# Kernel tuning notes

Measured on AMD Instinct MI355X. Metric: run time of the kernel, lower is better.

## Reference

```python
import jax, jax.numpy as jnp
import numpy as np

KH, KW = 3, 3
STRIDE, PAD, DIL = 1, 1, 1


def setup_inputs() -> dict:
    key = jax.random.key(0)
    k1, k2, k3, k4 = jax.random.split(key, 4)
    B, C, H, W = 4, 256, 64, 64
    O = 256
    x = jax.random.normal(k1, (B, C, H, W), dtype=jnp.float32)
    offset = jax.random.normal(k2, (B, 2 * KH * KW, H, W), dtype=jnp.float32)
    mask = jax.random.uniform(k3, (B, KH * KW, H, W), dtype=jnp.float32)
    weight = jax.random.normal(k4, (O, C, KH, KW), dtype=jnp.float32) * 0.02
    bias = jnp.zeros((O,), dtype=jnp.float32)
    return {"x": x, "offset": offset, "mask": mask, "weight": weight, "bias": bias}


def _bilinear_sample(x, py, px):
    # x: [B,C,H,W]; py,px: [B,K,Ho,Wo] fractional sample coords (zero outside)
    B, C, H, W = x.shape
    y0 = jnp.floor(py)
    x0 = jnp.floor(px)
    ly, lx = py - y0, px - x0
    hy, hx = 1.0 - ly, 1.0 - lx
    y0i = y0.astype(jnp.int32)
    x0i = x0.astype(jnp.int32)
    xf = x.reshape(B, C, H * W)

    def gather(yi, xi):
        valid = (yi >= 0) & (yi < H) & (xi >= 0) & (xi < W)
        yc = jnp.clip(yi, 0, H - 1)
        xc = jnp.clip(xi, 0, W - 1)
        idx = yc * W + xc  # [B,K,Ho,Wo]
        g = jax.vmap(lambda xb, ib: xb[:, ib.reshape(-1)])(xf, idx)  # [B,C,K*Ho*Wo]
        g = g.reshape(B, C, *yi.shape[1:])
        return g * valid[:, None].astype(x.dtype)

    return (gather(y0i, x0i) * (hy * hx)[:, None]
            + gather(y0i, x0i + 1) * (hy * lx)[:, None]
            + gather(y0i + 1, x0i) * (ly * hx)[:, None]
            + gather(y0i + 1, x0i + 1) * (ly * lx)[:, None])


def reference(x, offset, mask, weight, bias):
    B, C, H, W = x.shape
    O = weight.shape[0]
    K = KH * KW
    Ho = (H + 2 * PAD - DIL * (KH - 1) - 1) // STRIDE + 1
    Wo = (W + 2 * PAD - DIL * (KW - 1) - 1) // STRIDE + 1
    off = offset.reshape(B, K, 2, Ho, Wo)
    tap_y = (jnp.repeat(jnp.arange(KH), KW) * DIL).astype(x.dtype)  # [K]
    tap_x = (jnp.tile(jnp.arange(KW), KH) * DIL).astype(x.dtype)
    base_y = (jnp.arange(Ho) * STRIDE - PAD).astype(x.dtype)  # [Ho]
    base_x = (jnp.arange(Wo) * STRIDE - PAD).astype(x.dtype)
    py = off[:, :, 0] + base_y[None, None, :, None] + tap_y[None, :, None, None]
    px = off[:, :, 1] + base_x[None, None, None, :] + tap_x[None, :, None, None]
    # sampled columns: [B,C,K,Ho,Wo], modulated by mask
    val = _bilinear_sample(x, py, px) * mask[:, None]
    out = jnp.einsum('bckhw,ock->bohw', val, weight.reshape(O, C, K))
    return out + bias[None, :, None, None]
```

## Files before the change

### kernel.cpp

```cpp
#include <hip/hip_runtime.h>

typedef _Float16 f16x8 __attribute__((ext_vector_type(8)));
typedef float f32x4 __attribute__((ext_vector_type(4)));

__device__ __forceinline__ unsigned short f2h(float f) {
  union { _Float16 h; unsigned short u; } v;
  v.h = (_Float16)f;
  return v.u;
}
__device__ __forceinline__ f16x8 splat8(float w) {
  _Float16 h = (_Float16)w;
  f16x8 v = {h, h, h, h, h, h, h, h};
  return v;
}

__global__ __launch_bounds__(256) void prep_wx(
    const float* __restrict__ x, const float* __restrict__ w,
    unsigned short* __restrict__ xt, uint4* __restrict__ wfrag) {
  const int bid = blockIdx.x;
  const int t = threadIdx.x;
  if (bid >= 1024) {
    const int idx = (bid - 1024) * 256 + t;
    const int l = idx & 63;
    const int kt = (idx >> 6) % 72;
    const int g = idx / (72 * 64);
    const int o = g * 16 + (l & 15);
    const int kbase = kt * 32 + ((l >> 4) * 8);
    unsigned short h[8];
#pragma unroll
    for (int e = 0; e < 8; ++e) {
      const int klin = kbase + e;
      const int kk = klin >> 8;
      const int c = klin & 255;
      h[e] = f2h(w[((size_t)o * 256 + c) * 9 + kk]);
    }
    uint4 p;
    p.x = (unsigned)h[0] | ((unsigned)h[1] << 16);
    p.y = (unsigned)h[2] | ((unsigned)h[3] << 16);
    p.z = (unsigned)h[4] | ((unsigned)h[5] << 16);
    p.w = (unsigned)h[6] | ((unsigned)h[7] << 16);
    wfrag[idx] = p;
    return;
  }
  const int b = bid >> 8;
  const int h = (bid >> 2) & 63;
  const int cq = bid & 3;
  const int wave = t >> 6, lane = t & 63;
  __shared__ float lds[64][65];
  const int wpos = t >> 2, sub = t & 3;
  const int cl0 = wave * 4 + (lane >> 4);
  const int w0 = (lane & 15) * 4;
#pragma unroll
  for (int iter = 0; iter < 4; ++iter) {
    const int cl = iter * 16 + cl0;
    const int c = cq * 64 + cl;
    float4 v = *(const float4*)(x + (((size_t)b * 256 + c) * 64 + h) * 64 + w0);
    lds[cl][w0] = v.x; lds[cl][w0 + 1] = v.y;
    lds[cl][w0 + 2] = v.z; lds[cl][w0 + 3] = v.w;
  }
  __syncthreads();
  unsigned short hb[16];
#pragma unroll
  for (int j = 0; j < 16; ++j) hb[j] = f2h(lds[sub * 16 + j][wpos]);
  uint4 p0, p1;
  p0.x = (unsigned)hb[0] | ((unsigned)hb[1] << 16);
  p0.y = (unsigned)hb[2] | ((unsigned)hb[3] << 16);
  p0.z = (unsigned)hb[4] | ((unsigned)hb[5] << 16);
  p0.w = (unsigned)hb[6] | ((unsigned)hb[7] << 16);
  p1.x = (unsigned)hb[8] | ((unsigned)hb[9] << 16);
  p1.y = (unsigned)hb[10] | ((unsigned)hb[11] << 16);
  p1.z = (unsigned)hb[12] | ((unsigned)hb[13] << 16);
  p1.w = (unsigned)hb[14] | ((unsigned)hb[15] << 16);
  unsigned short* dst = xt + (((size_t)b * 64 + h) * 64 + wpos) * 256 + cq * 64 + sub * 16;
  *(uint4*)dst = p0;
  *(uint4*)(dst + 8) = p1;
}

__device__ __forceinline__ void combine8(uint4 q0, uint4 q1, uint4 q2, uint4 q3,
                                         float4 wt, _Float16* dst) {
  f16x8 t0, t1, t2, t3;
  __builtin_memcpy(&t0, &q0, 16);
  __builtin_memcpy(&t1, &q1, 16);
  __builtin_memcpy(&t2, &q2, 16);
  __builtin_memcpy(&t3, &q3, 16);
  f16x8 r = t0 * splat8(wt.x);
  r += t1 * splat8(wt.y);
  r += t2 * splat8(wt.z);
  r += t3 * splat8(wt.w);
  __builtin_memcpy(dst, &r, 16);
}

__global__ __launch_bounds__(512, 2) void dcn_fused(
    const unsigned short* __restrict__ xt, const float* __restrict__ off,
    const float* __restrict__ mask, const uint4* __restrict__ wfrag,
    const float* __restrict__ bias, float* __restrict__ out) {
  __shared__ __align__(16) _Float16 Bs[2][4096];
  __shared__ __align__(16) float swt[9 * 64 * 4];
  __shared__ __align__(16) int sidx[9 * 64 * 4];

  const int bid = blockIdx.x;
  const int id = ((bid & 7) << 5) | (bid >> 3);
  const int b = id >> 6;
  const int nt = id & 63;

  const int tid = threadIdx.x;
  const int lane = tid & 63;
  const int wv = tid >> 6;
  const int lh = lane & 15, lg = lane >> 4;

  for (int pair = tid; pair < 576; pair += 512) {
    const int k = pair >> 6;
    const int pl = pair & 63;
    float oy = off[(((size_t)b * 18 + 2 * k) * 64 + nt) * 64 + pl];
    float ox = off[(((size_t)b * 18 + 2 * k + 1) * 64 + nt) * 64 + pl];
    float m = mask[(((size_t)b * 9 + k) * 64 + nt) * 64 + pl];
    float py = oy + (float)(nt - 1 + k / 3);
    float px = ox + (float)(pl - 1 + k % 3);
    float y0f = floorf(py), x0f = floorf(px);
    float ly = py - y0f, lx = px - x0f;
    float hy = 1.f - ly, hx = 1.f - lx;
    int y0 = (int)y0f, x0 = (int)x0f;
    int y1 = y0 + 1, x1 = x0 + 1;
    bool vy0 = (y0 >= 0) && (y0 < 64);
    bool vy1 = (y1 >= 0) && (y1 < 64);
    bool vx0 = (x0 >= 0) && (x0 < 64);
    bool vx1 = (x1 >= 0) && (x1 < 64);
    int yc0 = min(max(y0, 0), 63), yc1 = min(max(y1, 0), 63);
    int xc0 = min(max(x0, 0), 63), xc1 = min(max(x1, 0), 63);
    int* sp = sidx + (k * 64 + pl) * 4;
    float* wp = swt + (k * 64 + pl) * 4;
    sp[0] = (yc0 * 64 + xc0) * 256;
    sp[1] = (yc0 * 64 + xc1) * 256;
    sp[2] = (yc1 * 64 + xc0) * 256;
    sp[3] = (yc1 * 64 + xc1) * 256;
    wp[0] = (vy0 && vx0) ? hy * hx * m : 0.f;
    wp[1] = (vy0 && vx1) ? hy * lx * m : 0.f;
    wp[2] = (vy1 && vx0) ? ly * hx * m : 0.f;
    wp[3] = (vy1 && vx1) ? ly * lx * m : 0.f;
  }

  const uint4* aBase = wfrag + (size_t)(wv * 2) * 72 * 64 + lane;

  const int pos = tid >> 3, ci = tid & 7;
  const unsigned short* xtb = xt + (size_t)b * 1048576 + ci * 8;
  const int bsw = (ci >> 2) * 2048 + pos * 32 + (((ci & 3) ^ ((pos >> 1) & 3)) * 8);

  const int csw = (lg ^ ((lh >> 1) & 3)) * 8;
  int boff[4];
#pragma unroll
  for (int fn = 0; fn < 4; ++fn) boff[fn] = (fn * 16 + lh) * 32 + csw;

#define LOADA(P, AR)                                                               \
  do {                                                                             \
    _Pragma("unroll") for (int j = 0; j < 4; ++j)                                  \
        AR[j] = aBase[(size_t)((((j & 1) * 72) + 2 * (P) + (j >> 1)) * 64)];       \
  } while (0)

#define LOADTAPS(Q0, Q1, Q2, Q3, IX, CO)                                           \
  do {                                                                             \
    Q0 = *(const uint4*)(xtb + (IX).x + (CO));                                     \
    Q1 = *(const uint4*)(xtb + (IX).y + (CO));                                     \
    Q2 = *(const uint4*)(xtb + (IX).z + (CO));                                     \
    Q3 = *(const uint4*)(xtb + (IX).w + (CO));                                     \
  } while (0)

#define MFMA_PHASE(BUF, AR)                                                        \
  do {                                                                             \
    const _Float16* Bb = &Bs[BUF][0];                                              \
    f16x8 b0[4], b1[4];                                                            \
    _Pragma("unroll") for (int fn = 0; fn < 4; ++fn) {                             \
      b0[fn] = *(const f16x8*)(Bb + boff[fn]);                                     \
      b1[fn] = *(const f16x8*)(Bb + 2048 + boff[fn]);                              \
    }                                                                              \
    __builtin_amdgcn_s_setprio(1);                                                 \
    _Pragma("unroll") for (int fm = 0; fm < 2; ++fm)                               \
        _Pragma("unroll") for (int fn = 0; fn < 4; ++fn) {                         \
      acc[fm][fn] = __builtin_amdgcn_mfma_f32_16x16x32_f16(                        \
          *(const f16x8*)&AR[fm], b0[fn], acc[fm][fn], 0, 0, 0);                   \
      acc[fm][fn] = __builtin_amdgcn_mfma_f32_16x16x32_f16(                        \
          *(const f16x8*)&AR[2 + fm], b1[fn], acc[fm][fn], 0, 0, 0);               \
    }                                                                              \
    __builtin_amdgcn_s_setprio(0);                                                 \
  } while (0)

#define BAR()                                                                      \
  do {                                                                             \
    asm volatile("s_waitcnt lgkmcnt(0)" ::: "memory");                             \
    __builtin_amdgcn_sched_barrier(0);                                             \
    __builtin_amdgcn_s_barrier();                                                  \
    __builtin_amdgcn_sched_barrier(0);                                             \
  } while (0)

#define PHASE(P_, AL, AC, QL0, QL1, QL2, QL3, QC0, QC1, QC2, QC3)                  \
  do {                                                                             \
    LOADA((P_) + 1, AL);                                                           \
    int4 ix = *(const int4*)(sidx + ((((P_) + 2) >> 2) * 64 + pos) * 4);           \
    LOADTAPS(QL0, QL1, QL2, QL3, ix, (((P_) + 2) & 3) * 64);                       \
    MFMA_PHASE((P_) & 1, AC);                                                      \
    float4 wt4 = *(const float4*)(swt + ((((P_) + 1) >> 2) * 64 + pos) * 4);       \
    combine8(QC0, QC1, QC2, QC3, wt4, &Bs[((P_) + 1) & 1][0] + bsw);               \
    BAR();                                                                         \
  } while (0)

  f32x4 acc[2][4] = {};
  uint4 AE[4], AO[4];
  uint4 qA0, qA1, qA2, qA3, qB0, qB1, qB2, qB3;

  __syncthreads();

  {
    float4 wt0 = *(const float4*)(swt + pos * 4);
    int4 ix0 = *(const int4*)(sidx + pos * 4);
    LOADTAPS(qA0, qA1, qA2, qA3, ix0, 0);
    combine8(qA0, qA1, qA2, qA3, wt0, &Bs[0][0] + bsw);
    LOADA(0, AE);
    LOADTAPS(qB0, qB1, qB2, qB3, ix0, 64);
    BAR();
  }

  for (int p = 0; p < 34; p += 2) {
    PHASE(p, AO, AE, qA0, qA1, qA2, qA3, qB0, qB1, qB2, qB3);
    PHASE(p + 1, AE, AO, qB0, qB1, qB2, qB3, qA0, qA1, qA2, qA3);
  }
  {
    LOADA(35, AO);
    float4 wt4 = *(const float4*)(swt + (8 * 64 + pos) * 4);
    MFMA_PHASE(0, AE);
    combine8(qB0, qB1, qB2, qB3, wt4, &Bs[1][0] + bsw);
    BAR();
    MFMA_PHASE(1, AO);
  }

  float* outb = out + (size_t)b * 1048576 + (size_t)nt * 64;
#pragma unroll
  for (int fm = 0; fm < 2; ++fm) {
#pragma unroll
    for (int i = 0; i < 4; ++i) {
      const int o = wv * 32 + fm * 16 + lg * 4 + i;
      const float bs = bias[o];
      float* orow = outb + (size_t)o * 4096 + lh;
#pragma unroll
      for (int fn = 0; fn < 4; ++fn) orow[fn * 16] = acc[fm][fn][i] + bs;
    }
  }
#undef LOADA
#undef LOADTAPS
#undef MFMA_PHASE
#undef BAR
#undef PHASE
}

extern "C" void kernel_launch(void* const* d_in, const int* in_sizes, int n_in,
                              void* d_out, int out_size, void* d_ws, size_t ws_size,
                              hipStream_t stream) {
  const float* x = (const float*)d_in[0];
  const float* off = (const float*)d_in[1];
  const float* mask = (const float*)d_in[2];
  const float* wgt = (const float*)d_in[3];
  const float* bias = (const float*)d_in[4];
  float* out = (float*)d_out;

  uint4* wfrag = (uint4*)d_ws;
  unsigned short* xtp = (unsigned short*)(wfrag + 73728);

  prep_wx<<<1312, 256, 0, stream>>>(x, wgt, xtp, wfrag);
  dcn_fused<<<256, 512, 0, stream>>>(xtp, off, mask, wfrag, bias, out);
}
```

Baseline: 45.98 us.

## Split K across wave halves with 64x64 warp tiles and LDS reduction

Changes the wave-to-tile mapping so that 4 waves each own 64 output channels and two wave groups split each K step. Each wave now loads one B fragment set and 4 A fragments instead of two B halves and 2x2 A fragments, which improves reuse of the B data read from LDS per MFMA. The partial sums are reduced through shared memory (dynamic, 68 KB) before the store. Extra costs are a larger accumulator register footprint, an LDS reduction pass with two barriers, and higher shared memory per block, which may hurt occupancy at 2 blocks per CU.

```diff
diff --git a/kernel.cpp b/kernel.cpp
--- a/kernel.cpp
+++ b/kernel.cpp
@@ -94,9 +94,11 @@
     const unsigned short* __restrict__ xt, const float* __restrict__ off,
     const float* __restrict__ mask, const uint4* __restrict__ wfrag,
     const float* __restrict__ bias, float* __restrict__ out) {
-  __shared__ __align__(16) _Float16 Bs[2][4096];
-  __shared__ __align__(16) float swt[9 * 64 * 4];
-  __shared__ __align__(16) int sidx[9 * 64 * 4];
+  extern __shared__ char smem[];
+  _Float16* Bs = (_Float16*)smem;
+  float* swt = (float*)(smem + 16384);
+  int* sidx = (int*)(smem + 25600);
+  float* red = (float*)smem;
 
   const int bid = blockIdx.x;
   const int id = ((bid & 7) << 5) | (bid >> 3);
@@ -106,6 +108,8 @@
   const int tid = threadIdx.x;
   const int lane = tid & 63;
   const int wv = tid >> 6;
+  const int m = wv & 3;
+  const int ks = wv >> 2;
   const int lh = lane & 15, lg = lane >> 4;
 
   for (int pair = tid; pair < 576; pair += 512) {
@@ -113,7 +117,7 @@
     const int pl = pair & 63;
     float oy = off[(((size_t)b * 18 + 2 * k) * 64 + nt) * 64 + pl];
     float ox = off[(((size_t)b * 18 + 2 * k + 1) * 64 + nt) * 64 + pl];
-    float m = mask[(((size_t)b * 9 + k) * 64 + nt) * 64 + pl];
+    float mk = mask[(((size_t)b * 9 + k) * 64 + nt) * 64 + pl];
     float py = oy + (float)(nt - 1 + k / 3);
     float px = ox + (float)(pl - 1 + k % 3);
     float y0f = floorf(py), x0f = floorf(px);
@@ -133,13 +137,13 @@
     sp[1] = (yc0 * 64 + xc1) * 256;
     sp[2] = (yc1 * 64 + xc0) * 256;
     sp[3] = (yc1 * 64 + xc1) * 256;
-    wp[0] = (vy0 && vx0) ? hy * hx * m : 0.f;
-    wp[1] = (vy0 && vx1) ? hy * lx * m : 0.f;
-    wp[2] = (vy1 && vx0) ? ly * hx * m : 0.f;
-    wp[3] = (vy1 && vx1) ? ly * lx * m : 0.f;
-  }
-
-  const uint4* aBase = wfrag + (size_t)(wv * 2) * 72 * 64 + lane;
+    wp[0] = (vy0 && vx0) ? hy * hx * mk : 0.f;
+    wp[1] = (vy0 && vx1) ? hy * lx * mk : 0.f;
+    wp[2] = (vy1 && vx0) ? ly * hx * mk : 0.f;
+    wp[3] = (vy1 && vx1) ? ly * lx * mk : 0.f;
+  }
+
+  const uint4* aBase = wfrag + (size_t)(m * 4) * 4608 + lane;
 
   const int pos = tid >> 3, ci = tid & 7;
   const unsigned short* xtb = xt + (size_t)b * 1048576 + ci * 8;
@@ -148,12 +152,12 @@
   const int csw = (lg ^ ((lh >> 1) & 3)) * 8;
   int boff[4];
 #pragma unroll
-  for (int fn = 0; fn < 4; ++fn) boff[fn] = (fn * 16 + lh) * 32 + csw;
+  for (int fn = 0; fn < 4; ++fn) boff[fn] = ks * 2048 + (fn * 16 + lh) * 32 + csw;
 
 #define LOADA(P, AR)                                                               \
   do {                                                                             \
     _Pragma("unroll") for (int j = 0; j < 4; ++j)                                  \
-        AR[j] = aBase[(size_t)((((j & 1) * 72) + 2 * (P) + (j >> 1)) * 64)];       \
+        AR[j] = aBase[(size_t)((j * 72 + 2 * (P) + ks) * 64)];                     \
   } while (0)
 
 #define LOADTAPS(Q0, Q1, Q2, Q3, IX, CO)                                           \
@@ -166,20 +170,15 @@
 
 #define MFMA_PHASE(BUF, AR)                                                        \
   do {                                                                             \
-    const _Float16* Bb = &Bs[BUF][0];                                              \
-    f16x8 b0[4], b1[4];                                                            \
-    _Pragma("unroll") for (int fn = 0; fn < 4; ++fn) {                             \
-      b0[fn] = *(const f16x8*)(Bb + boff[fn]);                                     \
-      b1[fn] = *(const f16x8*)(Bb + 2048 + boff[fn]);                              \
-    }                                                                              \
+    const _Float16* Bb = Bs + (BUF) * 4096;                                        \
+    f16x8 bv[4];                                                                   \
+    _Pragma("unroll") for (int fn = 0; fn < 4; ++fn)                               \
+        bv[fn] = *(const f16x8*)(Bb + boff[fn]);                                   \
     __builtin_amdgcn_s_setprio(1);                                                 \
-    _Pragma("unroll") for (int fm = 0; fm < 2; ++fm)                               \
-        _Pragma("unroll") for (int fn = 0; fn < 4; ++fn) {                         \
-      acc[fm][fn] = __builtin_amdgcn_mfma_f32_16x16x32_f16(                        \
-          *(const f16x8*)&AR[fm], b0[fn], acc[fm][fn], 0, 0, 0);                   \
-      acc[fm][fn] = __builtin_amdgcn_mfma_f32_16x16x32_f16(                        \
-          *(const f16x8*)&AR[2 + fm], b1[fn], acc[fm][fn], 0, 0, 0);               \
-    }                                                                              \
+    _Pragma("unroll") for (int fm = 0; fm < 4; ++fm)                               \
+        _Pragma("unroll") for (int fn = 0; fn < 4; ++fn)                           \
+            acc[fm][fn] = __builtin_amdgcn_mfma_f32_16x16x32_f16(                  \
+                *(const f16x8*)&AR[fm], bv[fn], acc[fm][fn], 0, 0, 0);             \
     __builtin_amdgcn_s_setprio(0);                                                 \
   } while (0)
 
@@ -196,13 +195,13 @@
     LOADA((P_) + 1, AL);                                                           \
     int4 ix = *(const int4*)(sidx + ((((P_) + 2) >> 2) * 64 + pos) * 4);           \
     LOADTAPS(QL0, QL1, QL2, QL3, ix, (((P_) + 2) & 3) * 64);                       \
+    float4 wt4 = *(const float4*)(swt + ((((P_) + 1) >> 2) * 64 + pos) * 4);       \
     MFMA_PHASE((P_) & 1, AC);                                                      \
-    float4 wt4 = *(const float4*)(swt + ((((P_) + 1) >> 2) * 64 + pos) * 4);       \
-    combine8(QC0, QC1, QC2, QC3, wt4, &Bs[((P_) + 1) & 1][0] + bsw);               \
+    combine8(QC0, QC1, QC2, QC3, wt4, Bs + (((P_) + 1) & 1) * 4096 + bsw);         \
     BAR();                                                                         \
   } while (0)
 
-  f32x4 acc[2][4] = {};
+  f32x4 acc[4][4] = {};
   uint4 AE[4], AO[4];
   uint4 qA0, qA1, qA2, qA3, qB0, qB1, qB2, qB3;
 
@@ -212,7 +211,7 @@
     float4 wt0 = *(const float4*)(swt + pos * 4);
     int4 ix0 = *(const int4*)(sidx + pos * 4);
     LOADTAPS(qA0, qA1, qA2, qA3, ix0, 0);
-    combine8(qA0, qA1, qA2, qA3, wt0, &Bs[0][0] + bsw);
+    combine8(qA0, qA1, qA2, qA3, wt0, Bs + bsw);
     LOADA(0, AE);
     LOADTAPS(qB0, qB1, qB2, qB3, ix0, 64);
     BAR();
@@ -226,22 +225,36 @@
     LOADA(35, AO);
     float4 wt4 = *(const float4*)(swt + (8 * 64 + pos) * 4);
     MFMA_PHASE(0, AE);
-    combine8(qB0, qB1, qB2, qB3, wt4, &Bs[1][0] + bsw);
+    combine8(qB0, qB1, qB2, qB3, wt4, Bs + 4096 + bsw);
     BAR();
     MFMA_PHASE(1, AO);
   }
 
-  float* outb = out + (size_t)b * 1048576 + (size_t)nt * 64;
-#pragma unroll
-  for (int fm = 0; fm < 2; ++fm) {
-#pragma unroll
-    for (int i = 0; i < 4; ++i) {
-      const int o = wv * 32 + fm * 16 + lg * 4 + i;
-      const float bs = bias[o];
-      float* orow = outb + (size_t)o * 4096 + lh;
-#pragma unroll
-      for (int fn = 0; fn < 4; ++fn) orow[fn * 16] = acc[fm][fn][i] + bs;
-    }
+  __syncthreads();
+  if (ks == 1) {
+#pragma unroll
+    for (int fm = 0; fm < 4; ++fm)
+#pragma unroll
+      for (int fn = 0; fn < 4; ++fn)
+#pragma unroll
+        for (int i = 0; i < 4; ++i)
+          red[(m * 64 + fm * 16 + lg * 4 + i) * 68 + fn * 16 + lh] = acc[fm][fn][i];
+  }
+  __syncthreads();
+  if (ks == 0) {
+    float* outb = out + (size_t)b * 1048576 + (size_t)nt * 64;
+#pragma unroll
+    for (int fm = 0; fm < 4; ++fm)
+#pragma unroll
+      for (int i = 0; i < 4; ++i) {
+        const int o = m * 64 + fm * 16 + lg * 4 + i;
+        const float bs = bias[o];
+        float* orow = outb + (size_t)o * 4096 + lh;
+        const float* rrow = red + (m * 64 + fm * 16 + lg * 4 + i) * 68 + lh;
+#pragma unroll
+        for (int fn = 0; fn < 4; ++fn)
+          orow[fn * 16] = acc[fm][fn][i] + rrow[fn * 16] + bs;
+      }
   }
 #undef LOADA
 #undef LOADTAPS
@@ -263,6 +276,10 @@
   uint4* wfrag = (uint4*)d_ws;
   unsigned short* xtp = (unsigned short*)(wfrag + 73728);
 
+  const int smem_bytes = 69632;
+  (void)hipFuncSetAttribute(reinterpret_cast<const void*>(&dcn_fused),
+                            hipFuncAttributeMaxDynamicSharedMemorySize, smem_bytes);
+
   prep_wx<<<1312, 256, 0, stream>>>(x, wgt, xtp, wfrag);
-  dcn_fused<<<256, 512, 0, stream>>>(xtp, off, mask, wfrag, bias, out);
-}
+  dcn_fused<<<256, 512, smem_bytes, stream>>>(xtp, off, mask, wfrag, bias, out);
+}
```

Result: no change. 45.69 us (-0.6%).
